# Kernel optimization log

Hardware: AMD Instinct MI355X
Metric: run time of the kernel (lower is better)

The kernel has to match this reference:

```python
import jax, jax.numpy as jnp
import numpy as np
import math

DIM = 256
B, T = 4, 4096

def setup_inputs() -> dict:
    key = jax.random.key(0)
    ks = jax.random.split(key, 16)
    d = DIM
    def lin(k, dout, din):
        bound = 1.0 / math.sqrt(din)
        kw, kb = jax.random.split(k)
        W = jax.random.uniform(kw, (dout, din), minval=-bound, maxval=bound, dtype=jnp.float32)
        b = jax.random.uniform(kb, (dout,), minval=-bound, maxval=bound, dtype=jnp.float32)
        return W, b
    x = jax.random.normal(ks[0], (B, T, d), dtype=jnp.float32)
    wq, bq = lin(ks[1], d, d)
    wk, bk = lin(ks[2], d, d)
    wv, bv = lin(ks[3], d, d)
    wo, bo = lin(ks[4], d, d)
    w1, b1 = lin(ks[5], 4 * d, d)
    w2, b2 = lin(ks[6], d, 4 * d)
    return {
        "x": x,
        "attn_norm_w": jnp.ones((d,), jnp.float32),
        "mlp_norm_w": jnp.ones((d,), jnp.float32),
        "wq": wq, "bq": bq, "wk": wk, "bk": bk, "wv": wv, "bv": bv,
        "wo": wo, "bo": bo, "w1": w1, "b1": b1, "w2": w2, "b2": b2,
    }

def _rms_norm(x, w, eps=1e-6):
    rms = jnp.sqrt(jnp.mean(x * x, axis=-1, keepdims=True) + eps)
    return x / rms * w

def reference(x, attn_norm_w, mlp_norm_w, wq, bq, wk, bk, wv, bv, wo, bo, w1, b1, w2, b2):
    b, t, d = x.shape
    xn = _rms_norm(x, attn_norm_w)
    q = xn @ wq.T + bq  # [b,t,d]
    k = xn @ wk.T + bk
    v = xn @ wv.T + bv
    scores = jnp.einsum('btd,bsd->bts', q, k) / math.sqrt(d)
    causal = jnp.tril(jnp.ones((t, t), dtype=bool))
    scores = jnp.where(causal, scores, -1e9)
    probs = jax.nn.softmax(scores, axis=-1)
    attn = jnp.einsum('bts,bsd->btd', probs, v)
    x = x + attn @ wo.T + bo
    hn = _rms_norm(x, mlp_norm_w)
    h = jax.nn.gelu(hn @ w1.T + b1, approximate=False)
    return x + h @ w2.T + b2
```

## Files before the change

### kernel.cpp

```cpp
#include <hip/hip_runtime.h>

typedef __attribute__((ext_vector_type(8))) short bfrag;
typedef __attribute__((ext_vector_type(4))) float f32x4;

__device__ __forceinline__ f32x4 mfma16(bfrag a, bfrag b, f32x4 c) {
    return __builtin_amdgcn_mfma_f32_16x16x32_bf16(a, b, c, 0, 0, 0);
}
__device__ __forceinline__ unsigned short f2bf(float f) {
    unsigned int u = __float_as_uint(f);
    u = u + 0x7fffu + ((u >> 16) & 1u);
    return (unsigned short)(u >> 16);
}
__device__ __forceinline__ void glds16(const unsigned short* g, unsigned short* l) {
    __builtin_amdgcn_global_load_lds(
        (const __attribute__((address_space(1))) void*)g,
        (__attribute__((address_space(3))) void*)l, 16, 0, 0);
}

#define DIM 256
#define BT  16384
#define TSEQ 4096
#define FB   1048576

__global__ __launch_bounds__(256) void k_prep(
    const float* __restrict__ x, const float* __restrict__ anw,
    const float* __restrict__ wq, const float* __restrict__ wk,
    const float* __restrict__ wv, const float* __restrict__ wo,
    const float* __restrict__ w1, const float* __restrict__ w2,
    unsigned short* __restrict__ wqb, unsigned short* __restrict__ wkb,
    unsigned short* __restrict__ wvb, unsigned short* __restrict__ wob,
    unsigned short* __restrict__ w1b, unsigned short* __restrict__ w2b,
    unsigned short* __restrict__ xn)
{
    int bid = blockIdx.x;
    if (bid < 768) {
        const float* src; unsigned short* dst; int base;
        if      (bid < 64)  { src = wq; dst = wqb; base = (bid      ) * 1024; }
        else if (bid < 128) { src = wk; dst = wkb; base = (bid - 64 ) * 1024; }
        else if (bid < 192) { src = wv; dst = wvb; base = (bid - 128) * 1024; }
        else if (bid < 256) { src = wo; dst = wob; base = (bid - 192) * 1024; }
        else if (bid < 512) { src = w1; dst = w1b; base = (bid - 256) * 1024; }
        else                { src = w2; dst = w2b; base = (bid - 512) * 1024; }
        int i = base + threadIdx.x * 4;
        float4 v = *(const float4*)(src + i);
        ushort4 o = make_ushort4(f2bf(v.x), f2bf(v.y), f2bf(v.z), f2bf(v.w));
        *(ushort4*)(dst + i) = o;
    } else {
        int row  = (bid - 768) * 4 + (threadIdx.x >> 6);
        int lane = threadIdx.x & 63;
        float4 v = *(const float4*)(x + row * DIM + lane * 4);
        float ss = v.x*v.x + v.y*v.y + v.z*v.z + v.w*v.w;
        #pragma unroll
        for (int off = 1; off < 64; off <<= 1) ss += __shfl_xor(ss, off);
        float inv = rsqrtf(ss * (1.0f / DIM) + 1e-6f);
        float4 w = *(const float4*)(anw + lane * 4);
        ushort4 o = make_ushort4(f2bf(v.x*inv*w.x), f2bf(v.y*inv*w.y),
                                 f2bf(v.z*inv*w.z), f2bf(v.w*inv*w.w));
        *(ushort4*)(xn + row * DIM + lane * 4) = o;
    }
}

__global__ __launch_bounds__(256) void k_qkv(
    const unsigned short* __restrict__ xn,
    const unsigned short* __restrict__ wqb, const unsigned short* __restrict__ wkb,
    const unsigned short* __restrict__ wvb,
    const float* __restrict__ bq, const float* __restrict__ bk, const float* __restrict__ bv,
    unsigned short* __restrict__ Q, unsigned short* __restrict__ KF,
    unsigned short* __restrict__ VF)
{
    int bid = blockIdx.x;
    int wave = threadIdx.x >> 6, lane = threadIdx.x & 63;
    int m0 = (bid / 3) * 64;
    int n0 = (bid % 3) * 256 + wave * 64;
    int wsel = n0 >> 8;
    int nc   = n0 & 255;
    const unsigned short* W = (wsel == 0) ? wqb : (wsel == 1) ? wkb : wvb;
    const float* bias       = (wsel == 0) ? bq  : (wsel == 1) ? bk  : bv;
    int q = lane >> 4, r = lane & 15;

    f32x4 acc[4][4] = {};
    for (int ks = 0; ks < 8; ++ks) {
        int koff = ks * 32 + q * 8;
        bfrag a[4], b[4];
        #pragma unroll
        for (int i = 0; i < 4; ++i) a[i] = *(const bfrag*)(xn + (m0 + i*16 + r) * DIM + koff);
        #pragma unroll
        for (int j = 0; j < 4; ++j) b[j] = *(const bfrag*)(W  + (nc + j*16 + r) * DIM + koff);
        #pragma unroll
        for (int i = 0; i < 4; ++i)
            #pragma unroll
            for (int j = 0; j < 4; ++j) acc[i][j] = mfma16(a[i], b[j], acc[i][j]);
    }

    if (wsel == 0) {
        #pragma unroll
        for (int j = 0; j < 4; ++j) {
            int col = nc + j * 16 + r;
            float bz = bias[col];
            #pragma unroll
            for (int i = 0; i < 4; ++i)
                #pragma unroll
                for (int g = 0; g < 4; ++g) {
                    int row = m0 + i * 16 + q * 4 + g;
                    Q[row * DIM + col] = f2bf(acc[i][j][g] + bz);
                }
        }
    } else if (wsel == 1) {
        #pragma unroll
        for (int j = 0; j < 4; ++j) {
            int col = nc + j * 16 + r;
            int ks = col >> 5, qc = (col >> 3) & 3, e = col & 7;
            float bz = bias[col];
            #pragma unroll
            for (int i = 0; i < 4; ++i)
                #pragma unroll
                for (int g = 0; g < 4; ++g) {
                    int row = m0 + i * 16 + q * 4 + g;
                    int bb = row >> 12;
                    int r5 = row & 31, tile = (row & 4095) >> 5;
                    int h = (r5 >> 2) & 1;
                    int rc = ((r5 >> 3) << 2) | (r5 & 3);
                    KF[bb * FB + (tile * 16 + ks * 2 + h) * 512 + (qc * 16 + rc) * 8 + e]
                        = f2bf(acc[i][j][g] + bz);
                }
        }
    } else {
        #pragma unroll
        for (int j = 0; j < 4; ++j) {
            int vd = nc + j * 16 + r;
            int jc = vd >> 4, rc = vd & 15;
            float bz = bias[vd];
            #pragma unroll
            for (int i = 0; i < 4; ++i) {
                int t0 = m0 + i * 16 + q * 4;
                int bb = t0 >> 12, tl = t0 & (TSEQ - 1);
                int tile = tl >> 5, qc = (tl >> 3) & 3, e0 = tl & 7;
                ushort4 o = make_ushort4(f2bf(acc[i][j][0] + bz), f2bf(acc[i][j][1] + bz),
                                         f2bf(acc[i][j][2] + bz), f2bf(acc[i][j][3] + bz));
                *(ushort4*)(VF + bb * FB + (tile * 16 + jc) * 512 + (qc * 16 + rc) * 8 + e0) = o;
            }
        }
    }
}

__global__ __launch_bounds__(128, 1) void k_attn(
    const unsigned short* __restrict__ Q, const unsigned short* __restrict__ KF,
    const unsigned short* __restrict__ VF, unsigned short* __restrict__ AO)
{
    __shared__ __align__(16) unsigned char arena[65536];
    int bid = blockIdx.x;
    int xcd = bid & 7;
    int batch = xcd >> 1;
    int qt = 255 - (((bid >> 3) << 1) | (xcd & 1));
    int wave = threadIdx.x >> 6;
    int lane = threadIdx.x & 63;
    int q = lane >> 4, r = lane & 15;
    int q0 = qt * 16;
    const unsigned short* Qb  = Q  + (size_t)batch * TSEQ * DIM;
    const unsigned short* KFb = KF + (size_t)batch * FB;
    const unsigned short* VFb = VF + (size_t)batch * FB;
    int lane8 = lane * 8;

    unsigned short* Kl = (unsigned short*)(arena + wave * 32768);
    unsigned short* Vl = Kl + 8192;

    bfrag qf[8];
    #pragma unroll
    for (int ks = 0; ks < 8; ++ks)
        qf[ks] = *(const bfrag*)(Qb + (q0 + r) * DIM + ks * 32 + q * 8);

    f32x4 o[16] = {};
    float lsum = 0.f;

    int ktiles = (q0 + 16 + 31) >> 5;
    int half = ktiles >> 1, rem = ktiles & 1;
    int cnt   = half + (wave == 0 ? rem : 0);
    int start = (wave == 0) ? 0 : half + rem;

    if (cnt > 0) {
        const unsigned short* kg = KFb + (size_t)start * 8192;
        #pragma unroll
        for (int f = 0; f < 16; ++f) glds16(kg + f * 512 + lane8, Kl + f * 512);
        const unsigned short* vg = VFb + (size_t)start * 8192;
        #pragma unroll
        for (int j = 0; j < 16; ++j) glds16(vg + j * 512 + lane8, Vl + j * 512);
    }

    for (int i = 0; i < cnt; ++i) {
        int kt = start + i;
        bool more = (i + 1 < cnt);
        asm volatile("s_waitcnt vmcnt(16)" ::: "memory");
        bfrag kb0[8], kb1[8];
        #pragma unroll
        for (int ks = 0; ks < 8; ++ks) {
            kb0[ks] = *(const bfrag*)(Kl + (ks * 2    ) * 512 + lane8);
            kb1[ks] = *(const bfrag*)(Kl + (ks * 2 + 1) * 512 + lane8);
        }
        f32x4 s0 = {}, s1 = {};
        #pragma unroll
        for (int ks = 0; ks < 8; ++ks) {
            s0 = mfma16(kb0[ks], qf[ks], s0);
            s1 = mfma16(kb1[ks], qf[ks], s1);
        }
        if (more) {
            asm volatile("s_waitcnt lgkmcnt(0)" ::: "memory");
            const unsigned short* kg = KFb + (size_t)(kt + 1) * 8192;
            #pragma unroll
            for (int f = 0; f < 16; ++f) glds16(kg + f * 512 + lane8, Kl + f * 512);
        }
        int kk0 = kt * 32;
        bool lastt = (kt == ktiles - 1);
        int qglob = q0 + r;
        bfrag pf;
        #pragma unroll
        for (int g = 0; g < 4; ++g) {
            int key0 = kk0 + q * 8 + g;
            float p0 = (lastt && key0     > qglob) ? 0.f : __expf(s0[g] * 0.0625f);
            float p1 = (lastt && key0 + 4 > qglob) ? 0.f : __expf(s1[g] * 0.0625f);
            lsum += p0 + p1;
            pf[g]     = (short)f2bf(p0);
            pf[g + 4] = (short)f2bf(p1);
        }
        if (more) asm volatile("s_waitcnt vmcnt(16)" ::: "memory");
        else      asm volatile("s_waitcnt vmcnt(0)"  ::: "memory");
        #pragma unroll
        for (int j = 0; j < 16; ++j) {
            bfrag vb = *(const bfrag*)(Vl + j * 512 + lane8);
            o[j] = mfma16(pf, vb, o[j]);
        }
        if (more) {
            asm volatile("s_waitcnt lgkmcnt(0)" ::: "memory");
            const unsigned short* vg = VFb + (size_t)(kt + 1) * 8192;
            #pragma unroll
            for (int j = 0; j < 16; ++j) glds16(vg + j * 512 + lane8, Vl + j * 512);
        }
    }

    lsum += __shfl_xor(lsum, 16);
    lsum += __shfl_xor(lsum, 32);
    __syncthreads();
    float* Obuf = (float*)arena;
    float* Lbuf = (float*)(arena + 16 * 260 * 4);
    if (wave == 0) {
        if (lane < 16) Lbuf[lane] = lsum;
        #pragma unroll
        for (int j = 0; j < 16; ++j)
            #pragma unroll
            for (int g = 0; g < 4; ++g)
                Obuf[(q * 4 + g) * 260 + j * 16 + r] = o[j][g];
    }
    __syncthreads();
    if (wave == 1) {
        if (lane < 16) Lbuf[lane] += lsum;
        #pragma unroll
        for (int j = 0; j < 16; ++j)
            #pragma unroll
            for (int g = 0; g < 4; ++g)
                Obuf[(q * 4 + g) * 260 + j * 16 + r] += o[j][g];
    }
    __syncthreads();

    float linv[4];
    #pragma unroll
    for (int g = 0; g < 4; ++g) linv[g] = 1.0f / Lbuf[q * 4 + g];
    unsigned short* Ob = AO + ((size_t)batch * TSEQ + q0) * DIM;
    #pragma unroll
    for (int jj = 0; jj < 8; ++jj) {
        int j = wave * 8 + jj;
        #pragma unroll
        for (int g = 0; g < 4; ++g)
            Ob[(q * 4 + g) * DIM + j * 16 + r] =
                f2bf(Obuf[(q * 4 + g) * 260 + j * 16 + r] * linv[g]);
    }
}

__global__ __launch_bounds__(256) void k_wo(
    const unsigned short* __restrict__ AO, const unsigned short* __restrict__ wob,
    const float* __restrict__ bo, const float* __restrict__ x,
    const float* __restrict__ mnw, float* __restrict__ x2,
    unsigned short* __restrict__ hn)
{
    int bid = blockIdx.x;
    int wave = threadIdx.x >> 6, lane = threadIdx.x & 63;
    int m0 = bid * 64 + wave * 16;
    int q = lane >> 4, r = lane & 15;
    f32x4 acc[16] = {};
    for (int ks = 0; ks < 8; ++ks) {
        int koff = ks * 32 + q * 8;
        bfrag a = *(const bfrag*)(AO + (m0 + r) * DIM + koff);
        #pragma unroll
        for (int j = 0; j < 16; ++j) {
            bfrag b = *(const bfrag*)(wob + (j * 16 + r) * DIM + koff);
            acc[j] = mfma16(a, b, acc[j]);
        }
    }
    float ss[4] = {0.f, 0.f, 0.f, 0.f};
    #pragma unroll
    for (int j = 0; j < 16; ++j) {
        int n = j * 16 + r;
        float bz = bo[n];
        #pragma unroll
        for (int g = 0; g < 4; ++g) {
            int row = m0 + q * 4 + g;
            float v = acc[j][g] + bz + x[row * DIM + n];
            acc[j][g] = v;
            ss[g] += v * v;
            x2[row * DIM + n] = v;
        }
    }
    #pragma unroll
    for (int g = 0; g < 4; ++g) {
        #pragma unroll
        for (int off = 1; off < 16; off <<= 1) ss[g] += __shfl_xor(ss[g], off);
    }
    #pragma unroll
    for (int j = 0; j < 16; ++j) {
        int n = j * 16 + r;
        float wn = mnw[n];
        #pragma unroll
        for (int g = 0; g < 4; ++g) {
            float inv = rsqrtf(ss[g] * (1.0f / DIM) + 1e-6f);
            hn[(m0 + q * 4 + g) * DIM + n] = f2bf(acc[j][g] * inv * wn);
        }
    }
}

__global__ __launch_bounds__(256) void k_w1(
    const unsigned short* __restrict__ hn, const unsigned short* __restrict__ w1b,
    const float* __restrict__ b1, unsigned short* __restrict__ h)
{
    int bid = blockIdx.x;
    int wave = threadIdx.x >> 6, lane = threadIdx.x & 63;
    int m0 = (bid >> 2) * 64;
    int n0 = (bid & 3) * 256 + wave * 64;
    int q = lane >> 4, r = lane & 15;
    f32x4 acc[4][4] = {};
    for (int ks = 0; ks < 8; ++ks) {
        int koff = ks * 32 + q * 8;
        bfrag a[4], b[4];
        #pragma unroll
        for (int i = 0; i < 4; ++i) a[i] = *(const bfrag*)(hn  + (m0 + i*16 + r) * DIM + koff);
        #pragma unroll
        for (int j = 0; j < 4; ++j) b[j] = *(const bfrag*)(w1b + (n0 + j*16 + r) * DIM + koff);
        #pragma unroll
        for (int i = 0; i < 4; ++i)
            #pragma unroll
            for (int j = 0; j < 4; ++j) acc[i][j] = mfma16(a[i], b[j], acc[i][j]);
    }
    #pragma unroll
    for (int j = 0; j < 4; ++j) {
        int n = n0 + j * 16 + r;
        float bz = b1[n];
        #pragma unroll
        for (int i = 0; i < 4; ++i)
            #pragma unroll
            for (int g = 0; g < 4; ++g) {
                int row = m0 + i * 16 + q * 4 + g;
                float v = acc[i][j][g] + bz;
                float ge = 0.5f * v * (1.0f + erff(v * 0.70710678118654752f));
                h[(size_t)row * 1024 + n] = f2bf(ge);
            }
    }
}

__global__ __launch_bounds__(256) void k_w2(
    const unsigned short* __restrict__ h, const unsigned short* __restrict__ w2b,
    const float* __restrict__ b2, const float* __restrict__ x2,
    float* __restrict__ out)
{
    int bid = blockIdx.x;
    int wave = threadIdx.x >> 6, lane = threadIdx.x & 63;
    int m0 = bid * 64;
    int n0 = wave * 64;
    int q = lane >> 4, r = lane & 15;
    f32x4 acc[4][4] = {};
    for (int ks = 0; ks < 32; ++ks) {
        int koff = ks * 32 + q * 8;
        bfrag a[4], b[4];
        #pragma unroll
        for (int i = 0; i < 4; ++i) a[i] = *(const bfrag*)(h   + (size_t)(m0 + i*16 + r) * 1024 + koff);
        #pragma unroll
        for (int j = 0; j < 4; ++j) b[j] = *(const bfrag*)(w2b + (size_t)(n0 + j*16 + r) * 1024 + koff);
        #pragma unroll
        for (int i = 0; i < 4; ++i)
            #pragma unroll
            for (int j = 0; j < 4; ++j) acc[i][j] = mfma16(a[i], b[j], acc[i][j]);
    }
    #pragma unroll
    for (int j = 0; j < 4; ++j) {
        int n = n0 + j * 16 + r;
        float bz = b2[n];
        #pragma unroll
        for (int i = 0; i < 4; ++i)
            #pragma unroll
            for (int g = 0; g < 4; ++g) {
                int row = m0 + i * 16 + q * 4 + g;
                out[row * DIM + n] = acc[i][j][g] + bz + x2[row * DIM + n];
            }
    }
}

#define OFF_WQB 0u
#define OFF_WKB 131072u
#define OFF_WVB 262144u
#define OFF_WOB 393216u
#define OFF_W1B 524288u
#define OFF_W2B 1048576u
#define OFF_XN  1572864u
#define OFF_Q   9961472u
#define OFF_KF  18350080u
#define OFF_VF  26738688u
#define OFF_AO  35127296u
#define OFF_X2  43515904u
#define OFF_HN  60293120u
#define OFF_H   OFF_XN

extern "C" void kernel_launch(void* const* d_in, const int* in_sizes, int n_in,
                              void* d_out, int out_size, void* d_ws, size_t ws_size,
                              hipStream_t stream) {
    const float* x   = (const float*)d_in[0];
    const float* anw = (const float*)d_in[1];
    const float* mnw = (const float*)d_in[2];
    const float* wq  = (const float*)d_in[3];
    const float* bq  = (const float*)d_in[4];
    const float* wk  = (const float*)d_in[5];
    const float* bk  = (const float*)d_in[6];
    const float* wv  = (const float*)d_in[7];
    const float* bv  = (const float*)d_in[8];
    const float* wo  = (const float*)d_in[9];
    const float* bo  = (const float*)d_in[10];
    const float* w1  = (const float*)d_in[11];
    const float* b1  = (const float*)d_in[12];
    const float* w2  = (const float*)d_in[13];
    const float* b2  = (const float*)d_in[14];
    float* out = (float*)d_out;

    char* ws = (char*)d_ws;
    unsigned short* wqb = (unsigned short*)(ws + OFF_WQB);
    unsigned short* wkb = (unsigned short*)(ws + OFF_WKB);
    unsigned short* wvb = (unsigned short*)(ws + OFF_WVB);
    unsigned short* wob = (unsigned short*)(ws + OFF_WOB);
    unsigned short* w1b = (unsigned short*)(ws + OFF_W1B);
    unsigned short* w2b = (unsigned short*)(ws + OFF_W2B);
    unsigned short* xn  = (unsigned short*)(ws + OFF_XN);
    unsigned short* Qp  = (unsigned short*)(ws + OFF_Q);
    unsigned short* KFp = (unsigned short*)(ws + OFF_KF);
    unsigned short* VFp = (unsigned short*)(ws + OFF_VF);
    unsigned short* AO  = (unsigned short*)(ws + OFF_AO);
    float*          x2  = (float*)         (ws + OFF_X2);
    unsigned short* hnp = (unsigned short*)(ws + OFF_HN);
    unsigned short* hp  = (unsigned short*)(ws + OFF_H);

    k_prep<<<dim3(4864), dim3(256), 0, stream>>>(x, anw, wq, wk, wv, wo, w1, w2,
                                                 wqb, wkb, wvb, wob, w1b, w2b, xn);
    k_qkv <<<dim3(768),  dim3(256), 0, stream>>>(xn, wqb, wkb, wvb, bq, bk, bv, Qp, KFp, VFp);
    k_attn<<<dim3(1024), dim3(128), 0, stream>>>(Qp, KFp, VFp, AO);
    k_wo  <<<dim3(256),  dim3(256), 0, stream>>>(AO, wob, bo, x, mnw, x2, hnp);
    k_w1  <<<dim3(1024), dim3(256), 0, stream>>>(hnp, w1b, b1, hp);
    k_w2  <<<dim3(256),  dim3(256), 0, stream>>>(hp, w2b, b2, x2, out);
}
```

Before: 336.8 us.

## Store GEMM operands in MFMA fragment-tiled layout for contiguous loads

```diff
diff --git a/kernel.cpp b/kernel.cpp
--- a/kernel.cpp
+++ b/kernel.cpp
@@ -21,33 +21,50 @@
 #define BT  16384
 #define TSEQ 4096
 #define FB   1048576
+
 
 __global__ __launch_bounds__(256) void k_prep(
     const float* __restrict__ x, const float* __restrict__ anw,
     const float* __restrict__ wq, const float* __restrict__ wk,
     const float* __restrict__ wv, const float* __restrict__ wo,
     const float* __restrict__ w1, const float* __restrict__ w2,
-    unsigned short* __restrict__ wqb, unsigned short* __restrict__ wkb,
-    unsigned short* __restrict__ wvb, unsigned short* __restrict__ wob,
-    unsigned short* __restrict__ w1b, unsigned short* __restrict__ w2b,
-    unsigned short* __restrict__ xn)
-{
-    int bid = blockIdx.x;
-    if (bid < 768) {
-        const float* src; unsigned short* dst; int base;
-        if      (bid < 64)  { src = wq; dst = wqb; base = (bid      ) * 1024; }
-        else if (bid < 128) { src = wk; dst = wkb; base = (bid - 64 ) * 1024; }
-        else if (bid < 192) { src = wv; dst = wvb; base = (bid - 128) * 1024; }
-        else if (bid < 256) { src = wo; dst = wob; base = (bid - 192) * 1024; }
-        else if (bid < 512) { src = w1; dst = w1b; base = (bid - 256) * 1024; }
-        else                { src = w2; dst = w2b; base = (bid - 512) * 1024; }
-        int i = base + threadIdx.x * 4;
-        float4 v = *(const float4*)(src + i);
-        ushort4 o = make_ushort4(f2bf(v.x), f2bf(v.y), f2bf(v.z), f2bf(v.w));
-        *(ushort4*)(dst + i) = o;
+    unsigned short* __restrict__ wqF, unsigned short* __restrict__ wkF,
+    unsigned short* __restrict__ wvF, unsigned short* __restrict__ woF,
+    unsigned short* __restrict__ w1F, unsigned short* __restrict__ w2F,
+    unsigned short* __restrict__ xnF)
+{
+    int bid = blockIdx.x;
+    int wave = threadIdx.x >> 6, lane = threadIdx.x & 63;
+    int q = lane >> 4, r = lane & 15;
+    if (bid < 384) {
+        int fid = bid * 4 + wave;
+        const float* src; unsigned short* dst; int ntile, ks, K, fbase;
+        if (fid < 512) {
+            int w = fid >> 7, fl = fid & 127;
+            ntile = fl >> 3; ks = fl & 7; K = 256;
+            src = (w == 0) ? wq : (w == 1) ? wk : (w == 2) ? wv : wo;
+            dst = (w == 0) ? wqF : (w == 1) ? wkF : (w == 2) ? wvF : woF;
+            fbase = (ntile * 8 + ks) * 512;
+        } else if (fid < 1024) {
+            int fl = fid - 512;
+            ntile = fl >> 3; ks = fl & 7; K = 256;
+            src = w1; dst = w1F;
+            fbase = (ntile * 8 + ks) * 512;
+        } else {
+            int fl = fid - 1024;
+            ntile = fl >> 5; ks = fl & 31; K = 1024;
+            src = w2; dst = w2F;
+            fbase = (ntile * 32 + ks) * 512;
+        }
+        const float* s = src + (ntile * 16 + r) * K + ks * 32 + q * 8;
+        float4 v0 = *(const float4*)(s);
+        float4 v1 = *(const float4*)(s + 4);
+        unsigned short o[8] = { f2bf(v0.x), f2bf(v0.y), f2bf(v0.z), f2bf(v0.w),
+                                f2bf(v1.x), f2bf(v1.y), f2bf(v1.z), f2bf(v1.w) };
+        *(ushort4*)(dst + fbase + lane * 8)     = make_ushort4(o[0], o[1], o[2], o[3]);
+        *(ushort4*)(dst + fbase + lane * 8 + 4) = make_ushort4(o[4], o[5], o[6], o[7]);
     } else {
-        int row  = (bid - 768) * 4 + (threadIdx.x >> 6);
-        int lane = threadIdx.x & 63;
+        int row  = (bid - 384) * 4 + wave;
         float4 v = *(const float4*)(x + row * DIM + lane * 4);
         float ss = v.x*v.x + v.y*v.y + v.z*v.z + v.w*v.w;
         #pragma unroll
@@ -56,14 +73,16 @@
         float4 w = *(const float4*)(anw + lane * 4);
         ushort4 o = make_ushort4(f2bf(v.x*inv*w.x), f2bf(v.y*inv*w.y),
                                  f2bf(v.z*inv*w.z), f2bf(v.w*inv*w.w));
-        *(ushort4*)(xn + row * DIM + lane * 4) = o;
+        int c = lane * 4;
+        int ks = c >> 5, qp = (c >> 3) & 3, e0 = c & 7;
+        *(ushort4*)(xnF + (((row >> 4) * 8 + ks) * 512) + ((qp * 16 + (row & 15)) * 8) + e0) = o;
     }
 }
 
 __global__ __launch_bounds__(256) void k_qkv(
-    const unsigned short* __restrict__ xn,
-    const unsigned short* __restrict__ wqb, const unsigned short* __restrict__ wkb,
-    const unsigned short* __restrict__ wvb,
+    const unsigned short* __restrict__ xnF,
+    const unsigned short* __restrict__ wqF, const unsigned short* __restrict__ wkF,
+    const unsigned short* __restrict__ wvF,
     const float* __restrict__ bq, const float* __restrict__ bk, const float* __restrict__ bv,
     unsigned short* __restrict__ Q, unsigned short* __restrict__ KF,
     unsigned short* __restrict__ VF)
@@ -74,18 +93,19 @@
     int n0 = (bid % 3) * 256 + wave * 64;
     int wsel = n0 >> 8;
     int nc   = n0 & 255;
-    const unsigned short* W = (wsel == 0) ? wqb : (wsel == 1) ? wkb : wvb;
-    const float* bias       = (wsel == 0) ? bq  : (wsel == 1) ? bk  : bv;
-    int q = lane >> 4, r = lane & 15;
+    const unsigned short* WF = (wsel == 0) ? wqF : (wsel == 1) ? wkF : wvF;
+    const float* bias        = (wsel == 0) ? bq  : (wsel == 1) ? bk  : bv;
+    int q = lane >> 4, r = lane & 15;
+    int lane8 = lane * 8;
+    int mt = m0 >> 4, nt = nc >> 4;
 
     f32x4 acc[4][4] = {};
     for (int ks = 0; ks < 8; ++ks) {
-        int koff = ks * 32 + q * 8;
         bfrag a[4], b[4];
         #pragma unroll
-        for (int i = 0; i < 4; ++i) a[i] = *(const bfrag*)(xn + (m0 + i*16 + r) * DIM + koff);
-        #pragma unroll
-        for (int j = 0; j < 4; ++j) b[j] = *(const bfrag*)(W  + (nc + j*16 + r) * DIM + koff);
+        for (int i = 0; i < 4; ++i) a[i] = *(const bfrag*)(xnF + ((mt + i) * 8 + ks) * 512 + lane8);
+        #pragma unroll
+        for (int j = 0; j < 4; ++j) b[j] = *(const bfrag*)(WF  + ((nt + j) * 8 + ks) * 512 + lane8);
         #pragma unroll
         for (int i = 0; i < 4; ++i)
             #pragma unroll
@@ -145,7 +165,7 @@
 
 __global__ __launch_bounds__(128, 1) void k_attn(
     const unsigned short* __restrict__ Q, const unsigned short* __restrict__ KF,
-    const unsigned short* __restrict__ VF, unsigned short* __restrict__ AO)
+    const unsigned short* __restrict__ VF, unsigned short* __restrict__ AOF)
 {
     __shared__ __align__(16) unsigned char arena[65536];
     int bid = blockIdx.x;
@@ -263,34 +283,37 @@
     float linv[4];
     #pragma unroll
     for (int g = 0; g < 4; ++g) linv[g] = 1.0f / Lbuf[q * 4 + g];
-    unsigned short* Ob = AO + ((size_t)batch * TSEQ + q0) * DIM;
+    unsigned short* AOt = AOF + (size_t)(batch * 256 + qt) * 8 * 512;
     #pragma unroll
     for (int jj = 0; jj < 8; ++jj) {
         int j = wave * 8 + jj;
+        int d = j * 16 + r;
+        int ks = d >> 5, qp = (d >> 3) & 3, e = d & 7;
         #pragma unroll
         for (int g = 0; g < 4; ++g)
-            Ob[(q * 4 + g) * DIM + j * 16 + r] =
+            AOt[ks * 512 + (qp * 16 + q * 4 + g) * 8 + e] =
                 f2bf(Obuf[(q * 4 + g) * 260 + j * 16 + r] * linv[g]);
     }
 }
 
 __global__ __launch_bounds__(256) void k_wo(
-    const unsigned short* __restrict__ AO, const unsigned short* __restrict__ wob,
+    const unsigned short* __restrict__ AOF, const unsigned short* __restrict__ woF,
     const float* __restrict__ bo, const float* __restrict__ x,
     const float* __restrict__ mnw, float* __restrict__ x2,
-    unsigned short* __restrict__ hn)
+    unsigned short* __restrict__ hnF)
 {
     int bid = blockIdx.x;
     int wave = threadIdx.x >> 6, lane = threadIdx.x & 63;
     int m0 = bid * 64 + wave * 16;
-    int q = lane >> 4, r = lane & 15;
+    int mt = bid * 4 + wave;
+    int q = lane >> 4, r = lane & 15;
+    int lane8 = lane * 8;
     f32x4 acc[16] = {};
     for (int ks = 0; ks < 8; ++ks) {
-        int koff = ks * 32 + q * 8;
-        bfrag a = *(const bfrag*)(AO + (m0 + r) * DIM + koff);
+        bfrag a = *(const bfrag*)(AOF + (mt * 8 + ks) * 512 + lane8);
         #pragma unroll
         for (int j = 0; j < 16; ++j) {
-            bfrag b = *(const bfrag*)(wob + (j * 16 + r) * DIM + koff);
+            bfrag b = *(const bfrag*)(woF + (j * 8 + ks) * 512 + lane8);
             acc[j] = mfma16(a, b, acc[j]);
         }
     }
@@ -316,32 +339,35 @@
     #pragma unroll
     for (int j = 0; j < 16; ++j) {
         int n = j * 16 + r;
+        int ks = n >> 5, qp = (n >> 3) & 3, e = n & 7;
         float wn = mnw[n];
         #pragma unroll
         for (int g = 0; g < 4; ++g) {
             float inv = rsqrtf(ss[g] * (1.0f / DIM) + 1e-6f);
-            hn[(m0 + q * 4 + g) * DIM + n] = f2bf(acc[j][g] * inv * wn);
+            hnF[(mt * 8 + ks) * 512 + (qp * 16 + q * 4 + g) * 8 + e]
+                = f2bf(acc[j][g] * inv * wn);
         }
     }
 }
 
 __global__ __launch_bounds__(256) void k_w1(
-    const unsigned short* __restrict__ hn, const unsigned short* __restrict__ w1b,
-    const float* __restrict__ b1, unsigned short* __restrict__ h)
+    const unsigned short* __restrict__ hnF, const unsigned short* __restrict__ w1F,
+    const float* __restrict__ b1, unsigned short* __restrict__ hF)
 {
     int bid = blockIdx.x;
     int wave = threadIdx.x >> 6, lane = threadIdx.x & 63;
     int m0 = (bid >> 2) * 64;
     int n0 = (bid & 3) * 256 + wave * 64;
-    int q = lane >> 4, r = lane & 15;
+    int mt = m0 >> 4, nt = n0 >> 4;
+    int q = lane >> 4, r = lane & 15;
+    int lane8 = lane * 8;
     f32x4 acc[4][4] = {};
     for (int ks = 0; ks < 8; ++ks) {
-        int koff = ks * 32 + q * 8;
         bfrag a[4], b[4];
         #pragma unroll
-        for (int i = 0; i < 4; ++i) a[i] = *(const bfrag*)(hn  + (m0 + i*16 + r) * DIM + koff);
-        #pragma unroll
-        for (int j = 0; j < 4; ++j) b[j] = *(const bfrag*)(w1b + (n0 + j*16 + r) * DIM + koff);
+        for (int i = 0; i < 4; ++i) a[i] = *(const bfrag*)(hnF + ((mt + i) * 8 + ks) * 512 + lane8);
+        #pragma unroll
+        for (int j = 0; j < 4; ++j) b[j] = *(const bfrag*)(w1F + ((nt + j) * 8 + ks) * 512 + lane8);
         #pragma unroll
         for (int i = 0; i < 4; ++i)
             #pragma unroll
@@ -350,21 +376,21 @@
     #pragma unroll
     for (int j = 0; j < 4; ++j) {
         int n = n0 + j * 16 + r;
+        int ks = n >> 5, qp = (n >> 3) & 3, e = n & 7;
         float bz = b1[n];
         #pragma unroll
         for (int i = 0; i < 4; ++i)
             #pragma unroll
             for (int g = 0; g < 4; ++g) {
-                int row = m0 + i * 16 + q * 4 + g;
                 float v = acc[i][j][g] + bz;
                 float ge = 0.5f * v * (1.0f + erff(v * 0.70710678118654752f));
-                h[(size_t)row * 1024 + n] = f2bf(ge);
+                hF[((mt + i) * 32 + ks) * 512 + (qp * 16 + q * 4 + g) * 8 + e] = f2bf(ge);
             }
     }
 }
 
 __global__ __launch_bounds__(256) void k_w2(
-    const unsigned short* __restrict__ h, const unsigned short* __restrict__ w2b,
+    const unsigned short* __restrict__ hF, const unsigned short* __restrict__ w2F,
     const float* __restrict__ b2, const float* __restrict__ x2,
     float* __restrict__ out)
 {
@@ -372,15 +398,16 @@
     int wave = threadIdx.x >> 6, lane = threadIdx.x & 63;
     int m0 = bid * 64;
     int n0 = wave * 64;
-    int q = lane >> 4, r = lane & 15;
+    int mt = m0 >> 4, nt = n0 >> 4;
+    int q = lane >> 4, r = lane & 15;
+    int lane8 = lane * 8;
     f32x4 acc[4][4] = {};
     for (int ks = 0; ks < 32; ++ks) {
-        int koff = ks * 32 + q * 8;
         bfrag a[4], b[4];
         #pragma unroll
-        for (int i = 0; i < 4; ++i) a[i] = *(const bfrag*)(h   + (size_t)(m0 + i*16 + r) * 1024 + koff);
-        #pragma unroll
-        for (int j = 0; j < 4; ++j) b[j] = *(const bfrag*)(w2b + (size_t)(n0 + j*16 + r) * 1024 + koff);
+        for (int i = 0; i < 4; ++i) a[i] = *(const bfrag*)(hF  + ((mt + i) * 32 + ks) * 512 + lane8);
+        #pragma unroll
+        for (int j = 0; j < 4; ++j) b[j] = *(const bfrag*)(w2F + ((nt + j) * 32 + ks) * 512 + lane8);
         #pragma unroll
         for (int i = 0; i < 4; ++i)
             #pragma unroll
@@ -436,26 +463,26 @@
     float* out = (float*)d_out;
 
     char* ws = (char*)d_ws;
-    unsigned short* wqb = (unsigned short*)(ws + OFF_WQB);
-    unsigned short* wkb = (unsigned short*)(ws + OFF_WKB);
-    unsigned short* wvb = (unsigned short*)(ws + OFF_WVB);
-    unsigned short* wob = (unsigned short*)(ws + OFF_WOB);
-    unsigned short* w1b = (unsigned short*)(ws + OFF_W1B);
-    unsigned short* w2b = (unsigned short*)(ws + OFF_W2B);
-    unsigned short* xn  = (unsigned short*)(ws + OFF_XN);
+    unsigned short* wqF = (unsigned short*)(ws + OFF_WQB);
+    unsigned short* wkF = (unsigned short*)(ws + OFF_WKB);
+    unsigned short* wvF = (unsigned short*)(ws + OFF_WVB);
+    unsigned short* woF = (unsigned short*)(ws + OFF_WOB);
+    unsigned short* w1F = (unsigned short*)(ws + OFF_W1B);
+    unsigned short* w2F = (unsigned short*)(ws + OFF_W2B);
+    unsigned short* xnF = (unsigned short*)(ws + OFF_XN);
     unsigned short* Qp  = (unsigned short*)(ws + OFF_Q);
     unsigned short* KFp = (unsigned short*)(ws + OFF_KF);
     unsigned short* VFp = (unsigned short*)(ws + OFF_VF);
-    unsigned short* AO  = (unsigned short*)(ws + OFF_AO);
+    unsigned short* AOF = (unsigned short*)(ws + OFF_AO);
     float*          x2  = (float*)         (ws + OFF_X2);
-    unsigned short* hnp = (unsigned short*)(ws + OFF_HN);
-    unsigned short* hp  = (unsigned short*)(ws + OFF_H);
-
-    k_prep<<<dim3(4864), dim3(256), 0, stream>>>(x, anw, wq, wk, wv, wo, w1, w2,
-                                                 wqb, wkb, wvb, wob, w1b, w2b, xn);
-    k_qkv <<<dim3(768),  dim3(256), 0, stream>>>(xn, wqb, wkb, wvb, bq, bk, bv, Qp, KFp, VFp);
-    k_attn<<<dim3(1024), dim3(128), 0, stream>>>(Qp, KFp, VFp, AO);
-    k_wo  <<<dim3(256),  dim3(256), 0, stream>>>(AO, wob, bo, x, mnw, x2, hnp);
-    k_w1  <<<dim3(1024), dim3(256), 0, stream>>>(hnp, w1b, b1, hp);
-    k_w2  <<<dim3(256),  dim3(256), 0, stream>>>(hp, w2b, b2, x2, out);
-}
+    unsigned short* hnF = (unsigned short*)(ws + OFF_HN);
+    unsigned short* hFp = (unsigned short*)(ws + OFF_H);
+
+    k_prep<<<dim3(4480), dim3(256), 0, stream>>>(x, anw, wq, wk, wv, wo, w1, w2,
+                                                 wqF, wkF, wvF, woF, w1F, w2F, xnF);
+    k_qkv <<<dim3(768),  dim3(256), 0, stream>>>(xnF, wqF, wkF, wvF, bq, bk, bv, Qp, KFp, VFp);
+    k_attn<<<dim3(1024), dim3(128), 0, stream>>>(Qp, KFp, VFp, AOF);
+    k_wo  <<<dim3(256),  dim3(256), 0, stream>>>(AOF, woF, bo, x, mnw, x2, hnF);
+    k_w1  <<<dim3(1024), dim3(256), 0, stream>>>(hnF, w1F, b1, hFp);
+    k_w2  <<<dim3(256),  dim3(256), 0, stream>>>(hFp, w2F, b2, x2, out);
+}
```

Measured after the change: 276.7 us. 1.22x faster.
